# Kernel optimization log

Measured on AMD Instinct MI355X. Metric: run time of the kernel, lower is better.

## Reference

```python
import jax, jax.numpy as jnp
import numpy as np

B, K, IN_DIM, H, D = 8, 4096, 512, 8, 64  # batch, tokens, in_dim, heads, per-head dim


def setup_inputs() -> dict:
    key = jax.random.key(0)
    ks = jax.random.split(key, 8)
    s = 0.02
    return {
        "x": jax.random.normal(ks[0], (B, K, IN_DIM), jnp.float32),
        "y": jax.random.normal(ks[1], (B, K, IN_DIM), jnp.float32),
        "Wq": jax.random.normal(ks[2], (IN_DIM, H * D), jnp.float32) * s,
        "bq": jnp.zeros((H * D,), jnp.float32),
        "Wk": jax.random.normal(ks[3], (IN_DIM, H * D), jnp.float32) * s,
        "bk": jnp.zeros((H * D,), jnp.float32),
        "Wv": jax.random.normal(ks[4], (IN_DIM, H * D), jnp.float32) * s,
        "bv": jnp.zeros((H * D,), jnp.float32),
        "Wp": jax.random.normal(ks[5], (IN_DIM, D), jnp.float32) * s,
        "gamma": jax.random.uniform(ks[6], (H, 1, 1, 1), jnp.float32) + 0.001,
    }


def _heads(t):
    # (B, K, H*D) -> (H, B, K, D); matches split_cat(t, D, dim=2, cat dim=0) head-major layout
    b, k, _ = t.shape
    return t.reshape(b, k, H, D).transpose(2, 0, 1, 3)


def reference(x, y, Wq, bq, Wk, bk, Wv, bv, Wp, gamma):
    q = _heads(x @ Wq + bq)   # (H,B,K,D)
    kk = _heads(x @ Wk + bk)  # (H,B,K,D)
    v = _heads(y @ Wv + bv)   # (H,B,K,D)
    # energy = q^T k contracted over tokens -> (H,B,D,D)
    energy = jnp.einsum('hbkd,hbke->hbde', q, kk)
    attn = jax.nn.softmax(energy, axis=-1)
    # out = v @ attn^T : out[k,q] = sum_e v[k,e] * attn[q,e]
    out = jnp.einsum('hbke,hbqe->hbkq', v, attn)  # (H,B,K,D)
    yp = y @ Wp  # projection(y): (B,K,D)
    out = (gamma * out + yp[None]) / (1.0 + gamma)
    return out.transpose(1, 0, 2, 3)  # (B,H,K,D)
```

## Files before the change

kernel.cpp:

```cpp
#include <hip/hip_runtime.h>

#define B_ 8
#define K_ 4096
#define IN_ 512
#define H_ 8
#define D_ 64
#define HD_ 512

typedef short bf16x8 __attribute__((ext_vector_type(8)));
typedef float f32x4 __attribute__((ext_vector_type(4)));
typedef unsigned short u16;
typedef unsigned short us8v __attribute__((ext_vector_type(8)));
typedef unsigned short us4v __attribute__((ext_vector_type(4)));

__device__ inline u16 f2bf_rn(float f) {
  unsigned u = __float_as_uint(f);
  u += 0x7fffu + ((u >> 16) & 1u);
  return (u16)(u >> 16);
}
__device__ inline float bf2f(u16 h) {
  return __uint_as_float(((unsigned)h) << 16);
}


__global__ __launch_bounds__(256) void k_cvt_x(const float* __restrict__ x,
                                               u16* __restrict__ xt_hi,
                                               u16* __restrict__ xt_lo,
                                               float* __restrict__ svec) {
  const int kt = blockIdx.x, ct = blockIdx.y, b = blockIdx.z;
  __shared__ float Xs[64][65];
  const int tid = threadIdx.x;
  const float* src = x + ((size_t)b * K_ + kt * 64) * IN_ + ct * 64;
#pragma unroll
  for (int r = 0; r < 4; ++r) {
    int idx = tid + 256 * r;
    int k = idx >> 4, c4 = (idx & 15) * 4;
    f32x4 v = *(const f32x4*)(src + (size_t)k * IN_ + c4);
    Xs[k][c4 + 0] = v[0];
    Xs[k][c4 + 1] = v[1];
    Xs[k][c4 + 2] = v[2];
    Xs[k][c4 + 3] = v[3];
  }
  __syncthreads();
  if (tid < 64) {
    float s = 0.f;
#pragma unroll
    for (int k = 0; k < 64; ++k) s += Xs[k][tid];
    atomicAdd(&svec[b * IN_ + ct * 64 + tid], s);
  }
#pragma unroll
  for (int r = 0; r < 2; ++r) {
    int idx = tid + 256 * r;
    int c = idx >> 3, ck = (idx & 7) * 8;
    us8v hv, lv;
#pragma unroll
    for (int j = 0; j < 8; ++j) {
      float f = Xs[ck + j][c];
      u16 h = f2bf_rn(f);
      float lo = f - bf2f(h);
      hv[j] = h;
      lv[j] = f2bf_rn(lo);
    }
    size_t off = ((size_t)(b * IN_ + ct * 64 + c)) * K_ + kt * 64 + ck;
    *(us8v*)(xt_hi + off) = hv;
    *(us8v*)(xt_lo + off) = lv;
  }
}

__global__ __launch_bounds__(256) void k_cvt_w(
    const float* __restrict__ Wq, const float* __restrict__ Wk,
    u16* __restrict__ Wqt_hi, u16* __restrict__ Wqt_lo,
    u16* __restrict__ Wkt_hi, u16* __restrict__ Wkt_lo) {
  const int ti = blockIdx.x, tj = blockIdx.y;
  const float* src = blockIdx.z ? Wk : Wq;
  u16* dhi = blockIdx.z ? Wkt_hi : Wqt_hi;
  u16* dlo = blockIdx.z ? Wkt_lo : Wqt_lo;
  __shared__ float T[64][65];
  const int tid = threadIdx.x;
#pragma unroll
  for (int r = 0; r < 4; ++r) {
    int idx = tid + 256 * r;
    int rr = idx >> 4, c4 = (idx & 15) * 4;
    f32x4 v = *(const f32x4*)(src + (size_t)(tj * 64 + rr) * 512 + ti * 64 + c4);
    T[rr][c4 + 0] = v[0]; T[rr][c4 + 1] = v[1];
    T[rr][c4 + 2] = v[2]; T[rr][c4 + 3] = v[3];
  }
  __syncthreads();
#pragma unroll
  for (int r = 0; r < 2; ++r) {
    int idx = tid + 256 * r;
    int d = idx >> 3, ck = (idx & 7) * 8;
    us8v hv, lv;
#pragma unroll
    for (int j = 0; j < 8; ++j) {
      float f = T[ck + j][d];
      u16 h = f2bf_rn(f);
      hv[j] = h;
      lv[j] = f2bf_rn(f - bf2f(h));
    }
    size_t off = (size_t)(ti * 64 + d) * 512 + tj * 64 + ck;
    *(us8v*)(dhi + off) = hv;
    *(us8v*)(dlo + off) = lv;
  }
}

#define GP 72

__global__ __launch_bounds__(256, 2) void k_gram_mfma(
    const u16* __restrict__ xt_hi, const u16* __restrict__ xt_lo,
    float* __restrict__ G) {
  int pp = blockIdx.x, ti = 0;
  while (pp >= 4 - ti) { pp -= 4 - ti; ++ti; }
  const int tj = ti + pp;
  const int b = blockIdx.y >> 3, kc = blockIdx.y & 7;
  __shared__ u16 Pih[128 * GP], Pil[128 * GP], Pjh[128 * GP], Pjl[128 * GP];
  const int tid = threadIdx.x;
  const int wave = tid >> 6, lane = tid & 63;
  const int wm = wave & 1, wn = wave >> 1;
  const int m16 = lane & 15, quad = lane >> 4;
  const size_t base_i = ((size_t)(b * IN_ + ti * 128)) * K_;
  const size_t base_j = ((size_t)(b * IN_ + tj * 128)) * K_;
  f32x4 zf = {0.f, 0.f, 0.f, 0.f};
  f32x4 acc[4][4];
#pragma unroll
  for (int mt = 0; mt < 4; ++mt)
#pragma unroll
    for (int nt = 0; nt < 4; ++nt) acc[mt][nt] = zf;
  const int kbeg = kc * 512, kend = kbeg + 512;
  for (int k0 = kbeg; k0 < kend; k0 += 64) {
    __syncthreads();
#pragma unroll
    for (int r = 0; r < 4; ++r) {
      int idx = tid + 256 * r;
      int row = idx >> 3, ck = (idx & 7) * 8;
      size_t gi = base_i + (size_t)row * K_ + k0 + ck;
      size_t gj = base_j + (size_t)row * K_ + k0 + ck;
      int lo = row * GP + ck;
      *(us8v*)&Pih[lo] = *(const us8v*)(xt_hi + gi);
      *(us8v*)&Pil[lo] = *(const us8v*)(xt_lo + gi);
      *(us8v*)&Pjh[lo] = *(const us8v*)(xt_hi + gj);
      *(us8v*)&Pjl[lo] = *(const us8v*)(xt_lo + gj);
    }
    __syncthreads();
#pragma unroll
    for (int kk = 0; kk < 64; kk += 32) {
      bf16x8 ah[4], al[4], bh[4], bl[4];
#pragma unroll
      for (int t = 0; t < 4; ++t) {
        int ar = (wm * 64 + t * 16 + m16) * GP + kk + quad * 8;
        ah[t] = *(const bf16x8*)&Pih[ar];
        al[t] = *(const bf16x8*)&Pil[ar];
        int br = (wn * 64 + t * 16 + m16) * GP + kk + quad * 8;
        bh[t] = *(const bf16x8*)&Pjh[br];
        bl[t] = *(const bf16x8*)&Pjl[br];
      }
#pragma unroll
      for (int mt = 0; mt < 4; ++mt)
#pragma unroll
        for (int nt = 0; nt < 4; ++nt) {
          acc[mt][nt] = __builtin_amdgcn_mfma_f32_16x16x32_bf16(
              ah[mt], bh[nt], acc[mt][nt], 0, 0, 0);
          acc[mt][nt] = __builtin_amdgcn_mfma_f32_16x16x32_bf16(
              ah[mt], bl[nt], acc[mt][nt], 0, 0, 0);
          acc[mt][nt] = __builtin_amdgcn_mfma_f32_16x16x32_bf16(
              al[mt], bh[nt], acc[mt][nt], 0, 0, 0);
        }
    }
  }
  float* Gb = G + (size_t)b * IN_ * IN_;
#pragma unroll
  for (int mt = 0; mt < 4; ++mt)
#pragma unroll
    for (int nt = 0; nt < 4; ++nt)
#pragma unroll
      for (int r = 0; r < 4; ++r) {
        int gi = ti * 128 + wm * 64 + mt * 16 + quad * 4 + r;
        int gj = tj * 128 + wn * 64 + nt * 16 + m16;
        atomicAdd(&Gb[(size_t)gi * IN_ + gj], acc[mt][nt][r]);
      }
}

__global__ __launch_bounds__(256) void k_cvt_g(const float* __restrict__ G,
                                               u16* __restrict__ Ghi,
                                               u16* __restrict__ Glo) {
  const int ti = blockIdx.x, tj = blockIdx.y, b = blockIdx.z;
  if (tj < ti) return;
  const float* Gb = G + (size_t)b * IN_ * IN_;
  u16* ghb = Ghi + (size_t)b * IN_ * IN_;
  u16* glb = Glo + (size_t)b * IN_ * IN_;
  __shared__ float T[64][65];
  const int tid = threadIdx.x;
#pragma unroll
  for (int r = 0; r < 4; ++r) {
    int idx = tid + 256 * r;
    int rr = idx >> 4, c4 = (idx & 15) * 4;
    f32x4 v = *(const f32x4*)(Gb + (size_t)(ti * 64 + rr) * IN_ + tj * 64 + c4);
    T[rr][c4 + 0] = v[0]; T[rr][c4 + 1] = v[1];
    T[rr][c4 + 2] = v[2]; T[rr][c4 + 3] = v[3];
  }
  __syncthreads();
#pragma unroll
  for (int r = 0; r < 2; ++r) {
    int idx = tid + 256 * r;
    int rr = idx >> 3, ck = (idx & 7) * 8;
    us8v hv, lv;
#pragma unroll
    for (int j = 0; j < 8; ++j) {
      float f = T[rr][ck + j];
      u16 h = f2bf_rn(f);
      hv[j] = h;
      lv[j] = f2bf_rn(f - bf2f(h));
    }
    size_t off = (size_t)(ti * 64 + rr) * IN_ + tj * 64 + ck;
    *(us8v*)(ghb + off) = hv;
    *(us8v*)(glb + off) = lv;
  }
  if (ti != tj) {
#pragma unroll
    for (int r = 0; r < 2; ++r) {
      int idx = tid + 256 * r;
      int rr = idx >> 3, ck = (idx & 7) * 8;
      us8v hv, lv;
#pragma unroll
      for (int j = 0; j < 8; ++j) {
        float f = T[ck + j][rr];
        u16 h = f2bf_rn(f);
        hv[j] = h;
        lv[j] = f2bf_rn(f - bf2f(h));
      }
      size_t off = (size_t)(tj * 64 + rr) * IN_ + ti * 64 + ck;
      *(us8v*)(ghb + off) = hv;
      *(us8v*)(glb + off) = lv;
    }
  }
}

__global__ __launch_bounds__(256) void k_aall_mfma(
    const u16* __restrict__ Wqt_hi, const u16* __restrict__ Wqt_lo,
    const u16* __restrict__ Ghi, const u16* __restrict__ Glo,
    u16* __restrict__ Ahi, u16* __restrict__ Alo) {
  const int ct = blockIdx.x;
  const int hb = blockIdx.y;
  const int h = hb >> 3, b = hb & 7;
  __shared__ u16 S[4 * 64 * GP];
  u16* Ah = S;
  u16* Al = S + 64 * GP;
  u16* Bh = S + 2 * 64 * GP;
  u16* Bl = S + 3 * 64 * GP;
  const int tid = threadIdx.x;
  const int wave = tid >> 6, lane = tid & 63;
  const int m16 = lane & 15, quad = lane >> 4;
  const u16* Abase_h = Wqt_hi + (size_t)(h * 64) * IN_;
  const u16* Abase_l = Wqt_lo + (size_t)(h * 64) * IN_;
  const u16* Bbase_h = Ghi + (size_t)b * IN_ * IN_ + (size_t)(ct * 64) * IN_;
  const u16* Bbase_l = Glo + (size_t)b * IN_ * IN_ + (size_t)(ct * 64) * IN_;
  f32x4 zf = {0.f, 0.f, 0.f, 0.f};
  f32x4 acc[4] = {zf, zf, zf, zf};
  for (int k0 = 0; k0 < IN_; k0 += 64) {
    __syncthreads();
#pragma unroll
    for (int r = 0; r < 2; ++r) {
      int idx = tid + 256 * r;
      int row = idx >> 3, ck = (idx & 7) * 8;
      int lo = row * GP + ck;
      *(us8v*)&Ah[lo] = *(const us8v*)(Abase_h + (size_t)row * IN_ + k0 + ck);
      *(us8v*)&Al[lo] = *(const us8v*)(Abase_l + (size_t)row * IN_ + k0 + ck);
      *(us8v*)&Bh[lo] = *(const us8v*)(Bbase_h + (size_t)row * IN_ + k0 + ck);
      *(us8v*)&Bl[lo] = *(const us8v*)(Bbase_l + (size_t)row * IN_ + k0 + ck);
    }
    __syncthreads();
#pragma unroll
    for (int kk = 0; kk < 64; kk += 32) {
      int arow = (wave * 16 + m16) * GP + kk + quad * 8;
      bf16x8 ah = *(const bf16x8*)&Ah[arow];
      bf16x8 al = *(const bf16x8*)&Al[arow];
#pragma unroll
      for (int n = 0; n < 4; ++n) {
        int brow = (n * 16 + m16) * GP + kk + quad * 8;
        bf16x8 bh = *(const bf16x8*)&Bh[brow];
        bf16x8 bl = *(const bf16x8*)&Bl[brow];
        acc[n] = __builtin_amdgcn_mfma_f32_16x16x32_bf16(ah, bh, acc[n], 0, 0, 0);
        acc[n] = __builtin_amdgcn_mfma_f32_16x16x32_bf16(ah, bl, acc[n], 0, 0, 0);
        acc[n] = __builtin_amdgcn_mfma_f32_16x16x32_bf16(al, bh, acc[n], 0, 0, 0);
      }
    }
  }
  __syncthreads();
  float* Sf = (float*)S;
#pragma unroll
  for (int n = 0; n < 4; ++n)
#pragma unroll
    for (int r = 0; r < 4; ++r) {
      int d = wave * 16 + quad * 4 + r;
      int cc = n * 16 + m16;
      Sf[d * 68 + cc] = acc[n][r];
    }
  __syncthreads();
#pragma unroll
  for (int r = 0; r < 2; ++r) {
    int idx = tid + 256 * r;
    int d = idx >> 3, ck = (idx & 7) * 8;
    us8v hv, lv;
#pragma unroll
    for (int j = 0; j < 8; ++j) {
      float f = Sf[d * 68 + ck + j];
      u16 h2 = f2bf_rn(f);
      hv[j] = h2;
      lv[j] = f2bf_rn(f - bf2f(h2));
    }
    size_t off = ((size_t)hb * 64 + d) * IN_ + ct * 64 + ck;
    *(us8v*)(Ahi + off) = hv;
    *(us8v*)(Alo + off) = lv;
  }
}

__global__ __launch_bounds__(256) void k_attn3(
    const u16* __restrict__ Ahi, const u16* __restrict__ Alo,
    const u16* __restrict__ Wqt_hi, const u16* __restrict__ Wqt_lo,
    const u16* __restrict__ Wkt_hi, const u16* __restrict__ Wkt_lo,
    const float* __restrict__ Wv, const float* __restrict__ Wp,
    const float* __restrict__ bq, const float* __restrict__ bk,
    const float* __restrict__ bv, const float* __restrict__ gamma,
    const float* __restrict__ svec, u16* __restrict__ Wft,
    float* __restrict__ bfin) {
  const int h = blockIdx.x, b = blockIdx.y;
  const int hb = h * B_ + b;
  const int tid = threadIdx.x;
  const int wave = tid >> 6, lane = tid & 63;
  const int m16 = lane & 15, quad = lane >> 4;
  __shared__ u16 S[4 * 64 * GP];
  __shared__ float Esh[64][65];
  __shared__ float t1[64], t2[64];
  u16* Ah = S;
  u16* Al = S + 64 * GP;
  u16* Bh = S + 2 * 64 * GP;
  u16* Bl = S + 3 * 64 * GP;

  if (tid < 64) {
    float s = 0.f;
    const u16* wh = Wkt_hi + (size_t)(h * 64 + tid) * IN_;
    const u16* wl = Wkt_lo + (size_t)(h * 64 + tid) * IN_;
    for (int c = 0; c < IN_; ++c)
      s += svec[b * IN_ + c] * (bf2f(wh[c]) + bf2f(wl[c]));
    t1[tid] = s;
  } else if (tid < 128) {
    int d = tid - 64;
    float s = 0.f;
    const u16* wh = Wqt_hi + (size_t)(h * 64 + d) * IN_;
    const u16* wl = Wqt_lo + (size_t)(h * 64 + d) * IN_;
    for (int c = 0; c < IN_; ++c)
      s += svec[b * IN_ + c] * (bf2f(wh[c]) + bf2f(wl[c]));
    t2[d] = s;
  }

  const u16* Abase_h = Ahi + (size_t)hb * 64 * IN_;
  const u16* Abase_l = Alo + (size_t)hb * 64 * IN_;
  const u16* Bbase_h = Wkt_hi + (size_t)(h * 64) * IN_;
  const u16* Bbase_l = Wkt_lo + (size_t)(h * 64) * IN_;
  f32x4 zf = {0.f, 0.f, 0.f, 0.f};
  f32x4 acc[4] = {zf, zf, zf, zf};
  for (int k0 = 0; k0 < IN_; k0 += 64) {
    __syncthreads();
#pragma unroll
    for (int r = 0; r < 2; ++r) {
      int idx = tid + 256 * r;
      int row = idx >> 3, ck = (idx & 7) * 8;
      int lo = row * GP + ck;
      *(us8v*)&Ah[lo] = *(const us8v*)(Abase_h + (size_t)row * IN_ + k0 + ck);
      *(us8v*)&Al[lo] = *(const us8v*)(Abase_l + (size_t)row * IN_ + k0 + ck);
      *(us8v*)&Bh[lo] = *(const us8v*)(Bbase_h + (size_t)row * IN_ + k0 + ck);
      *(us8v*)&Bl[lo] = *(const us8v*)(Bbase_l + (size_t)row * IN_ + k0 + ck);
    }
    __syncthreads();
#pragma unroll
    for (int kk = 0; kk < 64; kk += 32) {
      int arow = (wave * 16 + m16) * GP + kk + quad * 8;
      bf16x8 ah = *(const bf16x8*)&Ah[arow];
      bf16x8 al = *(const bf16x8*)&Al[arow];
#pragma unroll
      for (int n = 0; n < 4; ++n) {
        int brow = (n * 16 + m16) * GP + kk + quad * 8;
        bf16x8 bh = *(const bf16x8*)&Bh[brow];
        bf16x8 bl = *(const bf16x8*)&Bl[brow];
        acc[n] = __builtin_amdgcn_mfma_f32_16x16x32_bf16(ah, bh, acc[n], 0, 0, 0);
        acc[n] = __builtin_amdgcn_mfma_f32_16x16x32_bf16(ah, bl, acc[n], 0, 0, 0);
        acc[n] = __builtin_amdgcn_mfma_f32_16x16x32_bf16(al, bh, acc[n], 0, 0, 0);
      }
    }
  }
  __syncthreads();
#pragma unroll
  for (int n = 0; n < 4; ++n)
#pragma unroll
    for (int r = 0; r < 4; ++r) {
      int d = wave * 16 + quad * 4 + r;
      int e = n * 16 + m16;
      float bqd = bq[h * D_ + d], bke = bk[h * D_ + e];
      Esh[d][e] = acc[n][r] + bqd * t1[e] + t2[d] * bke + (float)K_ * bqd * bke;
    }
  __syncthreads();
  const float g = gamma[h];
  const float inv1g = 1.f / (1.f + g);
  if (tid < 64) {
    float m = -1e30f;
    for (int e = 0; e < 64; ++e) m = fmaxf(m, Esh[tid][e]);
    float ssum = 0.f;
    for (int e = 0; e < 64; ++e) {
      float p = __expf(Esh[tid][e] - m);
      Esh[tid][e] = p;
      ssum += p;
    }
    float inv = 1.f / ssum;
    float bsum = 0.f;
    for (int e = 0; e < 64; ++e) {
      Esh[tid][e] *= inv;
      bsum += bv[h * D_ + e] * Esh[tid][e];
    }
    bfin[hb * D_ + tid] = g * bsum * inv1g;
  }
  __syncthreads();

  bf16x8 bfr[4][2];
#pragma unroll
  for (int n = 0; n < 4; ++n)
#pragma unroll
    for (int kk = 0; kk < 2; ++kk)
#pragma unroll
      for (int j = 0; j < 8; ++j)
        bfr[n][kk][j] = f2bf_rn(Esh[n * 16 + m16][kk * 32 + quad * 8 + j]);

  u16* Wf = Wft + (size_t)hb * D_ * IN_;
#pragma unroll
  for (int mt = 0; mt < 8; ++mt) {
    f32x4 a4[4] = {zf, zf, zf, zf};
#pragma unroll
    for (int kk = 0; kk < 2; ++kk) {
      int c = wave * 128 + mt * 16 + m16;
      const float* wv = Wv + (size_t)c * HD_ + h * D_ + kk * 32 + quad * 8;
      f32x4 v0 = *(const f32x4*)wv;
      f32x4 v1 = *(const f32x4*)(wv + 4);
      bf16x8 af;
      af[0] = f2bf_rn(v0[0]); af[1] = f2bf_rn(v0[1]);
      af[2] = f2bf_rn(v0[2]); af[3] = f2bf_rn(v0[3]);
      af[4] = f2bf_rn(v1[0]); af[5] = f2bf_rn(v1[1]);
      af[6] = f2bf_rn(v1[2]); af[7] = f2bf_rn(v1[3]);
#pragma unroll
      for (int n = 0; n < 4; ++n)
        a4[n] = __builtin_amdgcn_mfma_f32_16x16x32_bf16(af, bfr[n][kk], a4[n], 0, 0, 0);
    }
    int cb = wave * 128 + mt * 16 + quad * 4;
#pragma unroll
    for (int n = 0; n < 4; ++n) {
      int q = n * 16 + m16;
      us4v st;
#pragma unroll
      for (int r = 0; r < 4; ++r) {
        float val = (g * a4[n][r] + Wp[(size_t)(cb + r) * D_ + q]) * inv1g;
        st[r] = f2bf_rn(val);
      }
      *(us4v*)(Wf + (size_t)q * IN_ + cb) = st;
    }
  }
}

__global__ __launch_bounds__(256, 4) void k_out_mfma(
    const float* __restrict__ y, const u16* __restrict__ Wft,
    const float* __restrict__ bfin, float* __restrict__ out) {
  const int kt = blockIdx.x;
  const int b = blockIdx.y & 7, hq = blockIdx.y >> 3;
  const int h0 = hq * 2;
  __shared__ u16 Wsh[2 * 64 * GP];
  const int tid = threadIdx.x, wave = tid >> 6, lane = tid & 63;
  const int m16 = lane & 15, quad = lane >> 4;
  f32x4 zf = {0.f, 0.f, 0.f, 0.f};
  f32x4 acc[2][2][4];
#pragma unroll
  for (int ms = 0; ms < 2; ++ms)
#pragma unroll
    for (int i = 0; i < 2; ++i)
#pragma unroll
      for (int nt = 0; nt < 4; ++nt) acc[ms][i][nt] = zf;
  for (int c0 = 0; c0 < IN_; c0 += 64) {
    __syncthreads();
#pragma unroll
    for (int r = 0; r < 4; ++r) {
      int idx = tid + 256 * r;
      int i = idx >> 9, q = (idx >> 3) & 63, ck = (idx & 7) * 8;
      const u16* src =
          Wft + ((size_t)((h0 + i) * 8 + b) * D_ + q) * IN_ + c0 + ck;
      *(us8v*)&Wsh[i * 64 * GP + q * GP + ck] = *(const us8v*)src;
    }
    __syncthreads();
#pragma unroll
    for (int kk = 0; kk < 2; ++kk) {
      bf16x8 af[2];
#pragma unroll
      for (int ms = 0; ms < 2; ++ms) {
        int row = kt * 128 + wave * 32 + ms * 16 + m16;
        const float* yp = y + ((size_t)b * K_ + row) * IN_ + c0 + kk * 32 + quad * 8;
        f32x4 v0 = *(const f32x4*)yp;
        f32x4 v1 = *(const f32x4*)(yp + 4);
        af[ms][0] = f2bf_rn(v0[0]); af[ms][1] = f2bf_rn(v0[1]);
        af[ms][2] = f2bf_rn(v0[2]); af[ms][3] = f2bf_rn(v0[3]);
        af[ms][4] = f2bf_rn(v1[0]); af[ms][5] = f2bf_rn(v1[1]);
        af[ms][6] = f2bf_rn(v1[2]); af[ms][7] = f2bf_rn(v1[3]);
      }
#pragma unroll
      for (int i = 0; i < 2; ++i)
#pragma unroll
        for (int nt = 0; nt < 4; ++nt) {
          bf16x8 bb = *(const bf16x8*)&Wsh[i * 64 * GP + (nt * 16 + m16) * GP +
                                           kk * 32 + quad * 8];
          acc[0][i][nt] =
              __builtin_amdgcn_mfma_f32_16x16x32_bf16(af[0], bb, acc[0][i][nt], 0, 0, 0);
          acc[1][i][nt] =
              __builtin_amdgcn_mfma_f32_16x16x32_bf16(af[1], bb, acc[1][i][nt], 0, 0, 0);
        }
    }
  }
#pragma unroll
  for (int i = 0; i < 2; ++i) {
    float* ob = out + (((size_t)b * H_ + h0 + i) * K_) * D_;
    const int hb = (h0 + i) * 8 + b;
#pragma unroll
    for (int ms = 0; ms < 2; ++ms)
#pragma unroll
      for (int nt = 0; nt < 4; ++nt) {
        int col = nt * 16 + m16;
        float bf = bfin[hb * D_ + col];
#pragma unroll
        for (int r = 0; r < 4; ++r) {
          int row = kt * 128 + wave * 32 + ms * 16 + quad * 4 + r;
          ob[(size_t)row * D_ + col] = acc[ms][i][nt][r] + bf;
        }
      }
  }
}

__global__ __launch_bounds__(256) void k_gram(const float* __restrict__ x,
                                              float* __restrict__ G,
                                              float* __restrict__ svec) {
  const int it = blockIdx.x, jt = blockIdx.y, b = blockIdx.z;
  if (jt < it) return;
  __shared__ float Xi[16][64];
  __shared__ float Xj[16][64];
  const float* Xb = x + (size_t)b * K_ * IN_;
  const int tx = threadIdx.x, ty = threadIdx.y;
  const int tid = ty * 16 + tx;
  const int i0 = it * 64, j0 = jt * 64;
  const bool diag = (it == jt);
  float acc[4][4] = {};
  float ssum = 0.f;
  for (int k0 = 0; k0 < K_; k0 += 16) {
#pragma unroll
    for (int r = 0; r < 4; ++r) {
      int idx = tid + 256 * r;
      int kk = idx >> 6, cc = idx & 63;
      const float* row = Xb + (size_t)(k0 + kk) * IN_;
      Xi[kk][cc] = row[i0 + cc];
      Xj[kk][cc] = row[j0 + cc];
    }
    __syncthreads();
#pragma unroll
    for (int kk = 0; kk < 16; ++kk) {
      float a[4], bb[4];
#pragma unroll
      for (int u = 0; u < 4; ++u) a[u] = Xi[kk][ty * 4 + u];
#pragma unroll
      for (int u = 0; u < 4; ++u) bb[u] = Xj[kk][tx * 4 + u];
#pragma unroll
      for (int u = 0; u < 4; ++u)
#pragma unroll
        for (int w = 0; w < 4; ++w) acc[u][w] += a[u] * bb[w];
    }
    if (diag && tid < 64) {
#pragma unroll
      for (int kk = 0; kk < 16; ++kk) ssum += Xi[kk][tid];
    }
    __syncthreads();
  }
  float* Gb = G + (size_t)b * IN_ * IN_;
#pragma unroll
  for (int u = 0; u < 4; ++u)
#pragma unroll
    for (int w = 0; w < 4; ++w) {
      int gi = i0 + ty * 4 + u, gj = j0 + tx * 4 + w;
      Gb[(size_t)gi * IN_ + gj] = acc[u][w];
      if (!diag) Gb[(size_t)gj * IN_ + gi] = acc[u][w];
    }
  if (diag && tid < 64) svec[b * IN_ + i0 + tid] = ssum;
}

__global__ __launch_bounds__(256) void k_aall(const float* __restrict__ Wq,
                                              const float* __restrict__ G,
                                              float* __restrict__ Aall) {
  const int jt = blockIdx.x;
  const int h = blockIdx.y, b = blockIdx.z;
  __shared__ float Ws[16][64];
  __shared__ float Gs[16][64];
  const float* Gb = G + (size_t)b * IN_ * IN_;
  const int tx = threadIdx.x, ty = threadIdx.y;
  const int tid = ty * 16 + tx;
  float acc[4][4] = {};
  for (int c0 = 0; c0 < IN_; c0 += 16) {
#pragma unroll
    for (int r = 0; r < 4; ++r) {
      int idx = tid + 256 * r;
      int kk = idx >> 6, cc = idx & 63;
      Ws[kk][cc] = Wq[(size_t)(c0 + kk) * HD_ + h * D_ + cc];
      Gs[kk][cc] = Gb[(size_t)(c0 + kk) * IN_ + jt * 64 + cc];
    }
    __syncthreads();
#pragma unroll
    for (int kk = 0; kk < 16; ++kk) {
      float a[4], bb[4];
#pragma unroll
      for (int u = 0; u < 4; ++u) a[u] = Ws[kk][ty * 4 + u];
#pragma unroll
      for (int u = 0; u < 4; ++u) bb[u] = Gs[kk][tx * 4 + u];
#pragma unroll
      for (int u = 0; u < 4; ++u)
#pragma unroll
        for (int w = 0; w < 4; ++w) acc[u][w] += a[u] * bb[w];
    }
    __syncthreads();
  }
  const int hb = h * B_ + b;
  float* Ahb = Aall + (size_t)hb * D_ * IN_;
#pragma unroll
  for (int u = 0; u < 4; ++u)
#pragma unroll
    for (int w = 0; w < 4; ++w)
      Ahb[(size_t)(ty * 4 + u) * IN_ + jt * 64 + tx * 4 + w] = acc[u][w];
}

__global__ __launch_bounds__(256) void k_attn_f32(
    const float* __restrict__ Wq, const float* __restrict__ Wk,
    const float* __restrict__ Wv, const float* __restrict__ Wp,
    const float* __restrict__ bq, const float* __restrict__ bk,
    const float* __restrict__ bv, const float* __restrict__ gamma,
    const float* __restrict__ Aall, const float* __restrict__ svec,
    float* __restrict__ Wfin, float* __restrict__ bfin) {
  const int h = blockIdx.x, b = blockIdx.y;
  const int hb = h * B_ + b;
  const int tx = threadIdx.x, ty = threadIdx.y;
  const int tid = ty * 16 + tx;
  __shared__ float Ast[64][17];
  __shared__ float Ws[16][64];
  __shared__ float Esh[64][65];
  __shared__ float t1[64], t2[64];
  const float* Ahb = Aall + (size_t)hb * D_ * IN_;
  if (tid < 64) {
    float a2 = 0.f;
    for (int c = 0; c < IN_; ++c)
      a2 += svec[b * IN_ + c] * Wk[(size_t)c * HD_ + h * D_ + tid];
    t1[tid] = a2;
  } else if (tid < 128) {
    int d = tid - 64;
    float a2 = 0.f;
    for (int c = 0; c < IN_; ++c)
      a2 += svec[b * IN_ + c] * Wq[(size_t)c * HD_ + h * D_ + d];
    t2[d] = a2;
  }
  float acc[4][4] = {};
  for (int c0 = 0; c0 < IN_; c0 += 16) {
#pragma unroll
    for (int r = 0; r < 4; ++r) {
      int idx = tid + 256 * r;
      int dd = idx >> 4, kk = idx & 15;
      Ast[dd][kk] = Ahb[(size_t)dd * IN_ + c0 + kk];
      int kk2 = idx >> 6, ee = idx & 63;
      Ws[kk2][ee] = Wk[(size_t)(c0 + kk2) * HD_ + h * D_ + ee];
    }
    __syncthreads();
#pragma unroll
    for (int kk = 0; kk < 16; ++kk) {
      float a[4], bb[4];
#pragma unroll
      for (int u = 0; u < 4; ++u) a[u] = Ast[ty * 4 + u][kk];
#pragma unroll
      for (int u = 0; u < 4; ++u) bb[u] = Ws[kk][tx * 4 + u];
#pragma unroll
      for (int u = 0; u < 4; ++u)
#pragma unroll
        for (int w = 0; w < 4; ++w) acc[u][w] += a[u] * bb[w];
    }
    __syncthreads();
  }
#pragma unroll
  for (int u = 0; u < 4; ++u) {
    int d = ty * 4 + u;
    float bqd = bq[h * D_ + d];
    float t2d = t2[d];
#pragma unroll
    for (int w = 0; w < 4; ++w) {
      int e = tx * 4 + w;
      float bke = bk[h * D_ + e];
      Esh[d][e] = acc[u][w] + bqd * t1[e] + t2d * bke + (float)K_ * bqd * bke;
    }
  }
  __syncthreads();
  if (tid < 64) {
    float m = -1e30f;
    for (int e = 0; e < 64; ++e) m = fmaxf(m, Esh[tid][e]);
    float ssum = 0.f;
    for (int e = 0; e < 64; ++e) {
      float p = __expf(Esh[tid][e] - m);
      Esh[tid][e] = p;
      ssum += p;
    }
    float inv = 1.f / ssum;
    for (int e = 0; e < 64; ++e) Esh[tid][e] *= inv;
  }
  __syncthreads();
  const float g = gamma[h];
  const float inv1g = 1.f / (1.f + g);
  if (tid < 64) {
    float a2 = 0.f;
    for (int e = 0; e < 64; ++e) a2 += bv[h * D_ + e] * Esh[tid][e];
    bfin[hb * D_ + tid] = g * a2 * inv1g;
  }
  float* Wf = Wfin + (size_t)hb * IN_ * D_;
  for (int it2 = 0; it2 < 128; ++it2) {
    int idx = tid + 256 * it2;
    int c = idx >> 6, q = idx & 63;
    const float* Wvr = Wv + (size_t)c * HD_ + h * D_;
    float a2 = 0.f;
#pragma unroll
    for (int e = 0; e < 64; ++e) a2 += Wvr[e] * Esh[q][e];
    Wf[idx] = (g * a2 + Wp[(size_t)c * D_ + q]) * inv1g;
  }
}

__global__ __launch_bounds__(256) void k_out_f32(const float* __restrict__ y,
                                                 const float* __restrict__ Wfin,
                                                 const float* __restrict__ bfin,
                                                 float* __restrict__ out) {
  const int kt = blockIdx.x;
  const int hb = blockIdx.y;
  const int h = hb >> 3, b = hb & 7;
  __shared__ float Ys[64][17];
  __shared__ float Ws[16][64];
  const int tx = threadIdx.x, ty = threadIdx.y;
  const int tid = ty * 16 + tx;
  const float* Yb = y + (size_t)b * K_ * IN_;
  const float* Wf = Wfin + (size_t)hb * IN_ * D_;
  const int k0 = kt * 64;
  float acc[4][4] = {};
  for (int c0 = 0; c0 < IN_; c0 += 16) {
#pragma unroll
    for (int r = 0; r < 4; ++r) {
      int idx = tid + 256 * r;
      int rr = idx >> 4, kk = idx & 15;
      Ys[rr][kk] = Yb[(size_t)(k0 + rr) * IN_ + c0 + kk];
      int kk2 = idx >> 6, qq = idx & 63;
      Ws[kk2][qq] = Wf[(size_t)(c0 + kk2) * D_ + qq];
    }
    __syncthreads();
#pragma unroll
    for (int kk = 0; kk < 16; ++kk) {
      float a[4], bb[4];
#pragma unroll
      for (int u = 0; u < 4; ++u) a[u] = Ys[ty * 4 + u][kk];
#pragma unroll
      for (int u = 0; u < 4; ++u) bb[u] = Ws[kk][tx * 4 + u];
#pragma unroll
      for (int u = 0; u < 4; ++u)
#pragma unroll
        for (int w = 0; w < 4; ++w) acc[u][w] += a[u] * bb[w];
    }
    __syncthreads();
  }
  float* ob = out + (((size_t)b * H_ + h) * K_ + k0) * D_;
#pragma unroll
  for (int u = 0; u < 4; ++u) {
    int k = ty * 4 + u;
#pragma unroll
    for (int w = 0; w < 4; ++w) {
      int q = tx * 4 + w;
      ob[(size_t)k * D_ + q] = acc[u][w] + bfin[hb * D_ + q];
    }
  }
}

extern "C" void kernel_launch(void* const* d_in, const int* in_sizes, int n_in,
                              void* d_out, int out_size, void* d_ws,
                              size_t ws_size, hipStream_t stream) {
  const float* x = (const float*)d_in[0];
  const float* y = (const float*)d_in[1];
  const float* Wq = (const float*)d_in[2];
  const float* bq = (const float*)d_in[3];
  const float* Wk = (const float*)d_in[4];
  const float* bk = (const float*)d_in[5];
  const float* Wv = (const float*)d_in[6];
  const float* bv = (const float*)d_in[7];
  const float* Wp = (const float*)d_in[8];
  const float* gm = (const float*)d_in[9];
  float* out = (float*)d_out;

  const size_t NEED = 86016000;
  if (ws_size >= NEED) {
    char* w = (char*)d_ws;
    u16* xt_hi = (u16*)(w);
    u16* Ahi = (u16*)(w);
    u16* Alo = (u16*)(w + 4194304);
    u16* Wft = (u16*)(w + 8388608);
    u16* xt_lo = (u16*)(w + 33554432);
    float* G = (float*)(w + 67108864);
    u16* Ghi = (u16*)(w + 75497472);
    u16* Glo = (u16*)(w + 79691776);
    u16* Wqt_hi = (u16*)(w + 83886080);
    u16* Wqt_lo = (u16*)(w + 84410368);
    u16* Wkt_hi = (u16*)(w + 84934656);
    u16* Wkt_lo = (u16*)(w + 85458944);
    float* bfin = (float*)(w + 85983232);
    float* svec = (float*)(w + 85999616);

    hipMemsetAsync(G, 0, 8388608, stream);
    hipMemsetAsync(svec, 0, 16384, stream);
    k_cvt_w<<<dim3(8, 8, 2), 256, 0, stream>>>(Wq, Wk, Wqt_hi, Wqt_lo, Wkt_hi,
                                               Wkt_lo);
    k_cvt_x<<<dim3(64, 8, 8), 256, 0, stream>>>(x, xt_hi, xt_lo, svec);
    k_gram_mfma<<<dim3(10, 64), 256, 0, stream>>>(xt_hi, xt_lo, G);
    k_cvt_g<<<dim3(8, 8, 8), 256, 0, stream>>>(G, Ghi, Glo);
    k_aall_mfma<<<dim3(8, 64), 256, 0, stream>>>(Wqt_hi, Wqt_lo, Ghi, Glo, Ahi,
                                                 Alo);
    k_attn3<<<dim3(8, 8), 256, 0, stream>>>(Ahi, Alo, Wqt_hi, Wqt_lo, Wkt_hi,
                                            Wkt_lo, Wv, Wp, bq, bk, bv, gm,
                                            svec, Wft, bfin);
    k_out_mfma<<<dim3(32, 32), 256, 0, stream>>>(y, Wft, bfin, out);
  } else {
    float* ws = (float*)d_ws;
    float* G = ws;
    float* Aall = ws + 2097152;
    float* Wfin = ws + 4194304;
    float* bfin = ws + 6291456;
    float* svec = ws + 6295552;
    dim3 blk(16, 16);
    k_gram<<<dim3(8, 8, 8), blk, 0, stream>>>(x, G, svec);
    k_aall<<<dim3(8, 8, 8), blk, 0, stream>>>(Wq, G, Aall);
    k_attn_f32<<<dim3(8, 8), blk, 0, stream>>>(Wq, Wk, Wv, Wp, bq, bk, bv, gm,
                                               Aall, svec, Wfin, bfin);
    k_out_f32<<<dim3(64, 64), blk, 0, stream>>>(y, Wfin, bfin, out);
  }
}
```

Baseline: 348.8 us.

## Pre-convert y to bf16, double-buffer and swizzle output GEMM, prefetch gram tiles

Adds a pass that converts y to bf16 once, so the output GEMM reads half the bytes and no longer repeats the conversion for every head pair. The output kernel now processes 256 rows per block with double-buffered, XOR-swizzled shared memory and register prefetch of the next y and W tiles. The gram kernel prefetches its next tile into registers while the MFMAs run. The cost is an extra kernel launch, a full pass over y, and higher register pressure (launch bounds drop to 2 blocks per CU).

```diff
diff --git a/kernel.cpp b/kernel.cpp
--- a/kernel.cpp
+++ b/kernel.cpp
@@ -65,6 +65,19 @@
     *(us8v*)(xt_hi + off) = hv;
     *(us8v*)(xt_lo + off) = lv;
   }
+}
+
+__global__ __launch_bounds__(256) void k_cvt_y(const float* __restrict__ y,
+                                               u16* __restrict__ yb) {
+  size_t i = ((size_t)blockIdx.x * 256 + threadIdx.x) * 8;
+  f32x4 v0 = *(const f32x4*)(y + i);
+  f32x4 v1 = *(const f32x4*)(y + i + 4);
+  us8v o;
+  o[0] = f2bf_rn(v0[0]); o[1] = f2bf_rn(v0[1]);
+  o[2] = f2bf_rn(v0[2]); o[3] = f2bf_rn(v0[3]);
+  o[4] = f2bf_rn(v1[0]); o[5] = f2bf_rn(v1[1]);
+  o[6] = f2bf_rn(v1[2]); o[7] = f2bf_rn(v1[3]);
+  *(us8v*)(yb + i) = o;
 }
 
 __global__ __launch_bounds__(256) void k_cvt_w(
@@ -127,21 +140,40 @@
 #pragma unroll
     for (int nt = 0; nt < 4; ++nt) acc[mt][nt] = zf;
   const int kbeg = kc * 512, kend = kbeg + 512;
-  for (int k0 = kbeg; k0 < kend; k0 += 64) {
-    __syncthreads();
+
+  us8v sih[4], sil[4], sjh[4], sjl[4];
+  auto GLOAD = [&](int k0) {
 #pragma unroll
     for (int r = 0; r < 4; ++r) {
       int idx = tid + 256 * r;
       int row = idx >> 3, ck = (idx & 7) * 8;
       size_t gi = base_i + (size_t)row * K_ + k0 + ck;
       size_t gj = base_j + (size_t)row * K_ + k0 + ck;
+      sih[r] = *(const us8v*)(xt_hi + gi);
+      sil[r] = *(const us8v*)(xt_lo + gi);
+      sjh[r] = *(const us8v*)(xt_hi + gj);
+      sjl[r] = *(const us8v*)(xt_lo + gj);
+    }
+  };
+  auto SWRITE = [&]() {
+#pragma unroll
+    for (int r = 0; r < 4; ++r) {
+      int idx = tid + 256 * r;
+      int row = idx >> 3, ck = (idx & 7) * 8;
       int lo = row * GP + ck;
-      *(us8v*)&Pih[lo] = *(const us8v*)(xt_hi + gi);
-      *(us8v*)&Pil[lo] = *(const us8v*)(xt_lo + gi);
-      *(us8v*)&Pjh[lo] = *(const us8v*)(xt_hi + gj);
-      *(us8v*)&Pjl[lo] = *(const us8v*)(xt_lo + gj);
-    }
-    __syncthreads();
+      *(us8v*)&Pih[lo] = sih[r];
+      *(us8v*)&Pil[lo] = sil[r];
+      *(us8v*)&Pjh[lo] = sjh[r];
+      *(us8v*)&Pjl[lo] = sjl[r];
+    }
+  };
+
+  GLOAD(kbeg);
+  SWRITE();
+  __syncthreads();
+  for (int k0 = kbeg; k0 < kend; k0 += 64) {
+    const bool more = (k0 + 64 < kend);
+    if (more) GLOAD(k0 + 64);
 #pragma unroll
     for (int kk = 0; kk < 64; kk += 32) {
       bf16x8 ah[4], al[4], bh[4], bl[4];
@@ -165,6 +197,11 @@
           acc[mt][nt] = __builtin_amdgcn_mfma_f32_16x16x32_bf16(
               al[mt], bh[nt], acc[mt][nt], 0, 0, 0);
         }
+    }
+    if (more) {
+      __syncthreads();
+      SWRITE();
+      __syncthreads();
     }
   }
   float* Gb = G + (size_t)b * IN_ * IN_;
@@ -463,74 +500,108 @@
   }
 }
 
-__global__ __launch_bounds__(256, 4) void k_out_mfma(
-    const float* __restrict__ y, const u16* __restrict__ Wft,
+__global__ __launch_bounds__(256, 2) void k_out_mfma(
+    const u16* __restrict__ yb, const u16* __restrict__ Wft,
     const float* __restrict__ bfin, float* __restrict__ out) {
   const int kt = blockIdx.x;
   const int b = blockIdx.y & 7, hq = blockIdx.y >> 3;
   const int h0 = hq * 2;
-  __shared__ u16 Wsh[2 * 64 * GP];
+  __shared__ u16 Wsh[2][2 * 64 * 64];
   const int tid = threadIdx.x, wave = tid >> 6, lane = tid & 63;
   const int m16 = lane & 15, quad = lane >> 4;
+  const int swz = (m16 & 7) << 3;
+
+  us8v stg[4];
+  auto LOAD = [&](int c0) {
+#pragma unroll
+    for (int r = 0; r < 4; ++r) {
+      int idx = tid + 256 * r;
+      int row = idx >> 3, ck = (idx & 7) * 8;
+      int i = row >> 6, q = row & 63;
+      const u16* src =
+          Wft + ((size_t)((h0 + i) * 8 + b) * 64 + q) * IN_ + c0 + ck;
+      stg[r] = *(const us8v*)src;
+    }
+  };
+  auto WRITE = [&](int buf) {
+#pragma unroll
+    for (int r = 0; r < 4; ++r) {
+      int idx = tid + 256 * r;
+      int row = idx >> 3, ck = (idx & 7) * 8;
+      *(us8v*)&Wsh[buf][row * 64 + (ck ^ ((row & 7) << 3))] = stg[r];
+    }
+  };
+  bf16x8 yf[2][4];
+  auto LOADY = [&](bf16x8 (*yd)[4], int c0) {
+#pragma unroll
+    for (int kk = 0; kk < 2; ++kk)
+#pragma unroll
+      for (int ms = 0; ms < 4; ++ms) {
+        int row = kt * 256 + wave * 64 + ms * 16 + m16;
+        yd[kk][ms] = *(const bf16x8*)(yb + ((size_t)b * K_ + row) * IN_ + c0 +
+                                      kk * 32 + quad * 8);
+      }
+  };
+
   f32x4 zf = {0.f, 0.f, 0.f, 0.f};
-  f32x4 acc[2][2][4];
-#pragma unroll
-  for (int ms = 0; ms < 2; ++ms)
+  f32x4 acc[4][2][4];
+#pragma unroll
+  for (int ms = 0; ms < 4; ++ms)
 #pragma unroll
     for (int i = 0; i < 2; ++i)
 #pragma unroll
       for (int nt = 0; nt < 4; ++nt) acc[ms][i][nt] = zf;
+
+  LOAD(0);
+  LOADY(yf, 0);
+  WRITE(0);
+  __syncthreads();
+  int cur = 0;
   for (int c0 = 0; c0 < IN_; c0 += 64) {
-    __syncthreads();
-#pragma unroll
-    for (int r = 0; r < 4; ++r) {
-      int idx = tid + 256 * r;
-      int i = idx >> 9, q = (idx >> 3) & 63, ck = (idx & 7) * 8;
-      const u16* src =
-          Wft + ((size_t)((h0 + i) * 8 + b) * D_ + q) * IN_ + c0 + ck;
-      *(us8v*)&Wsh[i * 64 * GP + q * GP + ck] = *(const us8v*)src;
-    }
-    __syncthreads();
-#pragma unroll
-    for (int kk = 0; kk < 2; ++kk) {
-      bf16x8 af[2];
-#pragma unroll
-      for (int ms = 0; ms < 2; ++ms) {
-        int row = kt * 128 + wave * 32 + ms * 16 + m16;
-        const float* yp = y + ((size_t)b * K_ + row) * IN_ + c0 + kk * 32 + quad * 8;
-        f32x4 v0 = *(const f32x4*)yp;
-        f32x4 v1 = *(const f32x4*)(yp + 4);
-        af[ms][0] = f2bf_rn(v0[0]); af[ms][1] = f2bf_rn(v0[1]);
-        af[ms][2] = f2bf_rn(v0[2]); af[ms][3] = f2bf_rn(v0[3]);
-        af[ms][4] = f2bf_rn(v1[0]); af[ms][5] = f2bf_rn(v1[1]);
-        af[ms][6] = f2bf_rn(v1[2]); af[ms][7] = f2bf_rn(v1[3]);
-      }
+    const bool more = (c0 + 64 < IN_);
+    bf16x8 yn[2][4];
+    if (more) {
+      LOAD(c0 + 64);
+      LOADY(yn, c0 + 64);
+    }
+#pragma unroll
+    for (int kk = 0; kk < 2; ++kk)
 #pragma unroll
       for (int i = 0; i < 2; ++i)
 #pragma unroll
         for (int nt = 0; nt < 4; ++nt) {
-          bf16x8 bb = *(const bf16x8*)&Wsh[i * 64 * GP + (nt * 16 + m16) * GP +
-                                           kk * 32 + quad * 8];
-          acc[0][i][nt] =
-              __builtin_amdgcn_mfma_f32_16x16x32_bf16(af[0], bb, acc[0][i][nt], 0, 0, 0);
-          acc[1][i][nt] =
-              __builtin_amdgcn_mfma_f32_16x16x32_bf16(af[1], bb, acc[1][i][nt], 0, 0, 0);
+          int brow = i * 64 + nt * 16 + m16;
+          bf16x8 bb = *(const bf16x8*)&Wsh[cur][brow * 64 +
+                                               ((kk * 32 + quad * 8) ^ swz)];
+#pragma unroll
+          for (int ms = 0; ms < 4; ++ms)
+            acc[ms][i][nt] = __builtin_amdgcn_mfma_f32_16x16x32_bf16(
+                yf[kk][ms], bb, acc[ms][i][nt], 0, 0, 0);
         }
-    }
-  }
+    if (more) {
+      WRITE(cur ^ 1);
+      __syncthreads();
+      cur ^= 1;
+#pragma unroll
+      for (int kk = 0; kk < 2; ++kk)
+#pragma unroll
+        for (int ms = 0; ms < 4; ++ms) yf[kk][ms] = yn[kk][ms];
+    }
+  }
+
 #pragma unroll
   for (int i = 0; i < 2; ++i) {
     float* ob = out + (((size_t)b * H_ + h0 + i) * K_) * D_;
     const int hb = (h0 + i) * 8 + b;
 #pragma unroll
-    for (int ms = 0; ms < 2; ++ms)
+    for (int ms = 0; ms < 4; ++ms)
 #pragma unroll
       for (int nt = 0; nt < 4; ++nt) {
         int col = nt * 16 + m16;
         float bf = bfin[hb * D_ + col];
 #pragma unroll
         for (int r = 0; r < 4; ++r) {
-          int row = kt * 128 + wave * 32 + ms * 16 + quad * 4 + r;
+          int row = kt * 256 + wave * 64 + ms * 16 + quad * 4 + r;
           ob[(size_t)row * D_ + col] = acc[ms][i][nt][r] + bf;
         }
       }
@@ -806,6 +877,7 @@
     u16* Alo = (u16*)(w + 4194304);
     u16* Wft = (u16*)(w + 8388608);
     u16* xt_lo = (u16*)(w + 33554432);
+    u16* yb = (u16*)(w + 33554432);
     float* G = (float*)(w + 67108864);
     u16* Ghi = (u16*)(w + 75497472);
     u16* Glo = (u16*)(w + 79691776);
@@ -822,13 +894,14 @@
                                                Wkt_lo);
     k_cvt_x<<<dim3(64, 8, 8), 256, 0, stream>>>(x, xt_hi, xt_lo, svec);
     k_gram_mfma<<<dim3(10, 64), 256, 0, stream>>>(xt_hi, xt_lo, G);
+    k_cvt_y<<<dim3(8192), 256, 0, stream>>>(y, yb);
     k_cvt_g<<<dim3(8, 8, 8), 256, 0, stream>>>(G, Ghi, Glo);
     k_aall_mfma<<<dim3(8, 64), 256, 0, stream>>>(Wqt_hi, Wqt_lo, Ghi, Glo, Ahi,
                                                  Alo);
     k_attn3<<<dim3(8, 8), 256, 0, stream>>>(Ahi, Alo, Wqt_hi, Wqt_lo, Wkt_hi,
                                             Wkt_lo, Wv, Wp, bq, bk, bv, gm,
                                             svec, Wft, bfin);
-    k_out_mfma<<<dim3(32, 32), 256, 0, stream>>>(y, Wft, bfin, out);
+    k_out_mfma<<<dim3(16, 32), 256, 0, stream>>>(yb, Wft, bfin, out);
   } else {
     float* ws = (float*)d_ws;
     float* G = ws;
```

After: 343.3 us. No clear change (-1.6%).
